# Optimization experiments

Hardware: AMD Instinct MI355X
Metric: run time of the kernel (lower is better)

## Reference

```python
import jax, jax.numpy as jnp
import numpy as np

B, S, H = 2, 2048, 2048
NH, G = 16, 4
HD = H // NH          # 128
REP = NH // G         # 4 query heads per KV group
KV = G * HD           # 512


def setup_inputs() -> dict:
    key = jax.random.key(0)
    ks = jax.random.split(key, 10)
    s = 0.02
    X = jax.random.normal(ks[0], (B, S, H), dtype=jnp.float32)
    Wq = jax.random.normal(ks[1], (H, H), dtype=jnp.float32) * s
    bq = jnp.zeros((H,), dtype=jnp.float32)
    Wk = jax.random.normal(ks[2], (H, KV), dtype=jnp.float32) * s
    bk = jnp.zeros((KV,), dtype=jnp.float32)
    Wv = jax.random.normal(ks[3], (H, KV), dtype=jnp.float32) * s
    bv = jnp.zeros((KV,), dtype=jnp.float32)
    Wo = jax.random.normal(ks[4], (H, H), dtype=jnp.float32) * s
    bo = jnp.zeros((H,), dtype=jnp.float32)
    # causal mask: 1 where attention is disallowed (strict upper triangle)
    casual_mask = jnp.triu(jnp.ones((S, S), dtype=jnp.float32), k=1)[None, None]
    return {"X": X, "Wq": Wq, "bq": bq, "Wk": Wk, "bk": bk,
            "Wv": Wv, "bv": bv, "Wo": Wo, "bo": bo,
            "casual_mask": casual_mask}


def reference(X, Wq, bq, Wk, bk, Wv, bv, Wo, bo, casual_mask):
    # projections
    q = X @ Wq + bq                          # [B,S,H]
    k = X @ Wk + bk                          # [B,S,G*HD]
    v = X @ Wv + bv                          # [B,S,G*HD]
    # split heads; q grouped as (group, rep) to match torch expand ordering
    q = q.reshape(B, S, NH, HD).transpose(0, 2, 1, 3)       # [B,NH,S,HD]
    q = q.reshape(B, G, REP, S, HD)                          # [B,G,REP,S,HD]
    k = k.reshape(B, S, G, HD).transpose(0, 2, 1, 3)         # [B,G,S,HD]
    v = v.reshape(B, S, G, HD).transpose(0, 2, 1, 3)         # [B,G,S,HD]
    scale = 1.0 / jnp.sqrt(jnp.float32(HD))
    scores = jnp.einsum('bgrqd,bgkd->bgrqk', q, k) * scale   # [B,G,REP,S,S]
    scores = scores + casual_mask * (-1e9)
    probs = jax.nn.softmax(scores, axis=-1)
    out = jnp.einsum('bgrqk,bgkd->bgrqd', probs, v)          # [B,G,REP,S,HD]
    out = out.reshape(B, NH, S, HD).transpose(0, 2, 1, 3).reshape(B, S, H)
    return out @ Wo + bo
```

## Files before the change

kernel.cpp:

```cpp
#include <hip/hip_runtime.h>

#define B_   2
#define S_   2048
#define H_   2048
#define NH_  16
#define G_   4
#define HD_  128
#define KV_  512
#define HQKV 3072

typedef __attribute__((ext_vector_type(8))) short bf16x8;
typedef __attribute__((ext_vector_type(4))) float f32x4;

__device__ __forceinline__ unsigned short f2bf(float f) {
    unsigned u = __float_as_uint(f);
    u += 0x7fff + ((u >> 16) & 1);
    return (unsigned short)(u >> 16);
}
__device__ __forceinline__ float bf2f(unsigned short s) {
    return __uint_as_float(((unsigned)s) << 16);
}

#define GLDS16(gsrc, ldst)                                                            \
    __builtin_amdgcn_global_load_lds(                                                 \
        (const __attribute__((address_space(1))) void*)(gsrc),                        \
        (__attribute__((address_space(3))) void*)(ldst), 16, 0, 0)

#define SC2F (0.08838834764831843f * 1.4426950408889634f)

__global__ void k_cvt_bf16(const float* __restrict__ in, unsigned short* __restrict__ out, int n4) {
    int i = blockIdx.x * blockDim.x + threadIdx.x;
    if (i >= n4) return;
    float4 v = ((const float4*)in)[i];
    ushort4 o;
    o.x = f2bf(v.x); o.y = f2bf(v.y); o.z = f2bf(v.z); o.w = f2bf(v.w);
    ((ushort4*)out)[i] = o;
}

__global__ void k_transpose_cvt(const float* __restrict__ in, unsigned short* __restrict__ out,
                                int R, int C) {
    __shared__ float t[32][33];
    int c0 = blockIdx.x * 32, r0 = blockIdx.y * 32;
    int tx = threadIdx.x, ty = threadIdx.y;
#pragma unroll
    for (int i = 0; i < 4; ++i)
        t[ty + i*8][tx] = in[(size_t)(r0 + ty + i*8) * C + c0 + tx];
    __syncthreads();
#pragma unroll
    for (int i = 0; i < 4; ++i)
        out[(size_t)(c0 + ty + i*8) * R + r0 + tx] = f2bf(t[tx][ty + i*8]);
}

__global__ void k_concat_bias(const float* __restrict__ bq, const float* __restrict__ bk,
                              const float* __restrict__ bv, float* __restrict__ out) {
    int i = blockIdx.x * 256 + threadIdx.x;
    if (i >= HQKV) return;
    out[i] = (i < H_) ? bq[i] : (i < H_ + KV_ ? bk[i - H_] : bv[i - H_ - KV_]);
}

__global__ void k_transpose_v(const unsigned short* __restrict__ in, unsigned short* __restrict__ out) {
    __shared__ unsigned short t[32][33];
    int b = blockIdx.z;
    int c0 = blockIdx.x * 32, s0 = blockIdx.y * 32;
    int tx = threadIdx.x, ty = threadIdx.y;
#pragma unroll
    for (int i = 0; i < 4; ++i)
        t[ty + i*8][tx] = in[((size_t)b * S_ + s0 + ty + i*8) * HQKV + (H_ + KV_) + c0 + tx];
    __syncthreads();
#pragma unroll
    for (int i = 0; i < 4; ++i)
        out[((size_t)b * KV_ + c0 + ty + i*8) * S_ + s0 + tx] = t[tx][ty + i*8];
}

template <bool BF16OUT, bool QSCALE>
__global__ __launch_bounds__(256) void k_gemm_bt(
    const unsigned short* __restrict__ A, const unsigned short* __restrict__ Bt,
    const float* __restrict__ bias, void* __restrict__ Cout, int M, int N, int K) {
    __shared__ __align__(16) unsigned short As[128 * 64];
    __shared__ __align__(16) unsigned short Bs[128 * 64];
    const int tid = threadIdx.x, lane = tid & 63, w = tid >> 6;
    const int l15 = lane & 15, l4 = lane >> 4;
    const int wr = w >> 1, wc = w & 1;
    const int m0 = blockIdx.x * 128, n0 = blockIdx.y * 128;
    f32x4 acc[4][4] = {};

    for (int kt = 0; kt < K; kt += 64) {
        __syncthreads();
#pragma unroll
        for (int i = 0; i < 4; ++i) {
            int p = (w * 4 + i) * 64 + lane;
            int row = p >> 3, c = (p & 7) ^ (row & 7);
            GLDS16(A + (size_t)(m0 + row) * K + kt + c * 8, As + (size_t)(w * 4 + i) * 512);
        }
#pragma unroll
        for (int i = 0; i < 4; ++i) {
            int p = (w * 4 + i) * 64 + lane;
            int row = p >> 3, c = (p & 7) ^ (row & 7);
            GLDS16(Bt + (size_t)(n0 + row) * K + kt + c * 8, Bs + (size_t)(w * 4 + i) * 512);
        }
        __syncthreads();
#pragma unroll
        for (int ks = 0; ks < 2; ++ks) {
            bf16x8 af[4], bfr[4];
#pragma unroll
            for (int m = 0; m < 4; ++m) {
                int row = wr * 64 + m * 16 + l15;
                int ch = (ks * 4 + l4) ^ (row & 7);
                af[m] = *(const bf16x8*)(As + row * 64 + ch * 8);
            }
#pragma unroll
            for (int n = 0; n < 4; ++n) {
                int row = wc * 64 + n * 16 + l15;
                int ch = (ks * 4 + l4) ^ (row & 7);
                bfr[n] = *(const bf16x8*)(Bs + row * 64 + ch * 8);
            }
#pragma unroll
            for (int m = 0; m < 4; ++m)
#pragma unroll
                for (int n = 0; n < 4; ++n)
                    acc[m][n] = __builtin_amdgcn_mfma_f32_16x16x32_bf16(af[m], bfr[n], acc[m][n], 0, 0, 0);
        }
    }
#pragma unroll
    for (int m = 0; m < 4; ++m) {
        int row = m0 + wr * 64 + m * 16 + l4 * 4;
#pragma unroll
        for (int n = 0; n < 4; ++n) {
            int col = n0 + wc * 64 + n * 16 + l15;
            float bv = bias[col];
#pragma unroll
            for (int r = 0; r < 4; ++r) {
                float v = acc[m][n][r] + bv;
                if (QSCALE) { if (col < H_) v *= SC2F; }
                if (BF16OUT)
                    ((unsigned short*)Cout)[(size_t)(row + r) * N + col] = f2bf(v);
                else
                    ((float*)Cout)[(size_t)(row + r) * N + col] = v;
            }
        }
    }
}

__global__ __launch_bounds__(256, 4) void k_flash(
    const unsigned short* __restrict__ QKV,
    const unsigned short* __restrict__ VT,
    unsigned short* __restrict__ Oa,
    unsigned short* __restrict__ part1,
    float* __restrict__ mlbuf) {
    __shared__ __align__(16) unsigned short Ks[64 * 128];
    __shared__ __align__(16) unsigned short Vs[128 * 64];
    __shared__ __align__(16) unsigned short Ps[4][16][36];
    const int tid = threadIdx.x, lane = tid & 63, w = tid >> 6;
    const int l15 = lane & 15, l4 = lane >> 4;
    const int bid = blockIdx.x;
    const int xcd = bid & 7, idx = bid >> 3;
    const int bh = xcd * 4 + (idx & 3);
    const int jidx = idx >> 2;
    const int b = bh >> 4, nh = bh & 15, g = nh >> 2;

    int qt, t0, t1, mode;
    if (jidx < 16) { qt = 16 + jidx; t0 = 0; t1 = 16; mode = 1; }
    else {
        int k = jidx - 16, j = k >> 1;
        if ((k & 1) == 0) { qt = 31 - j; t0 = 16; t1 = qt + 1; mode = 2; }
        else              { qt = 15 - j; t0 = 0;  t1 = qt + 1; mode = 0; }
    }
    const int qbase = qt * 64 + w * 16;

    const unsigned short* kgbase = QKV + (size_t)b * S_ * HQKV + H_ + g * HD_;
    const unsigned short* vgbase = VT + ((size_t)b * KV_ + g * HD_) * S_;

    auto issueK = [&](int kt) {
        const int kv0 = kt * 64;
#pragma unroll
        for (int i = 0; i < 4; ++i) {
            int p = i * 256 + tid;
            int row = p >> 4, c = (p & 15) ^ (row & 15);
            GLDS16(kgbase + (size_t)(kv0 + row) * HQKV + c * 8, &Ks[(i * 256 + w * 64) * 8]);
        }
    };
    auto issueV = [&](int kt) {
        const int kv0 = kt * 64;
#pragma unroll
        for (int i = 0; i < 4; ++i) {
            int p = i * 256 + tid;
            int row = p >> 3, c = (p & 7) ^ (row & 7);
            GLDS16(vgbase + (size_t)row * S_ + kv0 + c * 8, &Vs[(i * 256 + w * 64) * 8]);
        }
    };

    bf16x8 qf[4];
#pragma unroll
    for (int kb = 0; kb < 4; ++kb)
        qf[kb] = *(const bf16x8*)(QKV + (size_t)(b * S_ + qbase + l15) * HQKV +
                                  nh * HD_ + kb * 32 + l4 * 8);

    f32x4 o[8] = {};
    float mrow[4], lrow[4];
#pragma unroll
    for (int r = 0; r < 4; ++r) { mrow[r] = -1e30f; lrow[r] = 0.f; }

    issueK(t0);
    issueV(t0);

    for (int kt = t0; kt < t1; ++kt) {
        const int kv0 = kt * 64;
        asm volatile("s_waitcnt vmcnt(4)" ::: "memory");
        __builtin_amdgcn_s_barrier();
        __builtin_amdgcn_sched_barrier(0);

        f32x4 s[4] = {};
#pragma unroll
        for (int kb = 0; kb < 4; ++kb) {
            bf16x8 kf[4];
#pragma unroll
            for (int n = 0; n < 4; ++n) {
                int row = n * 16 + l15;
                int sl = (kb * 4 + l4) ^ (row & 15);
                kf[n] = *(const bf16x8*)(&Ks[(row * 16 + sl) * 8]);
            }
#pragma unroll
            for (int n = 0; n < 4; ++n)
                s[n] = __builtin_amdgcn_mfma_f32_16x16x32_bf16(qf[kb], kf[n], s[n], 0, 0, 0);
        }
        if (kv0 + 63 > qbase) {
#pragma unroll
            for (int n = 0; n < 4; ++n)
#pragma unroll
                for (int r = 0; r < 4; ++r) {
                    int kcol = kv0 + n * 16 + l15;
                    int qrow = qbase + l4 * 4 + r;
                    if (kcol > qrow) s[n][r] = -1e30f;
                }
        }
        float vm[4];
#pragma unroll
        for (int r = 0; r < 4; ++r) {
            float v = fmaxf(fmaxf(s[0][r], s[1][r]), fmaxf(s[2][r], s[3][r]));
            v = fmaxf(v, __shfl_xor(v, 1));
            v = fmaxf(v, __shfl_xor(v, 2));
            v = fmaxf(v, __shfl_xor(v, 4));
            v = fmaxf(v, __shfl_xor(v, 8));
            vm[r] = v;
        }
        int needs = 0;
#pragma unroll
        for (int r = 0; r < 4; ++r) needs |= (vm[r] > mrow[r] + 8.0f) ? 1 : 0;
        if (__any(needs)) {
            float sf[4];
#pragma unroll
            for (int r = 0; r < 4; ++r) {
                float mn = fmaxf(mrow[r], vm[r]);
                sf[r] = exp2f(mrow[r] - mn);
                mrow[r] = mn;
                lrow[r] *= sf[r];
            }
#pragma unroll
            for (int nc = 0; nc < 8; ++nc) {
                f32x4 t = o[nc];
                t[0] *= sf[0]; t[1] *= sf[1]; t[2] *= sf[2]; t[3] *= sf[3];
                o[nc] = t;
            }
        }
        float rs[4] = {0.f, 0.f, 0.f, 0.f};
#pragma unroll
        for (int n = 0; n < 4; ++n)
#pragma unroll
            for (int r = 0; r < 4; ++r) {
                float p = exp2f(s[n][r] - mrow[r]);
                s[n][r] = p;
                rs[r] += p;
            }
#pragma unroll
        for (int r = 0; r < 4; ++r) {
            float t = rs[r];
            t += __shfl_xor(t, 1); t += __shfl_xor(t, 2);
            t += __shfl_xor(t, 4); t += __shfl_xor(t, 8);
            lrow[r] += t;
        }

        asm volatile("s_waitcnt vmcnt(0)" ::: "memory");
        __builtin_amdgcn_s_barrier();
        __builtin_amdgcn_sched_barrier(0);
        if (kt + 1 < t1) issueK(kt + 1);

#pragma unroll
        for (int h = 0; h < 2; ++h) {
#pragma unroll
            for (int n = 0; n < 2; ++n)
#pragma unroll
                for (int r = 0; r < 4; ++r)
                    Ps[w][l4 * 4 + r][n * 16 + l15] = f2bf(s[2 * h + n][r]);
            bf16x8 pf = *(const bf16x8*)(&Ps[w][l15][l4 * 8]);
#pragma unroll
            for (int nc = 0; nc < 8; ++nc) {
                int row = nc * 16 + l15;
                int sl = (h * 4 + l4) ^ (row & 7);
                bf16x8 vf = *(const bf16x8*)(&Vs[(row * 8 + sl) * 8]);
                o[nc] = __builtin_amdgcn_mfma_f32_16x16x32_bf16(pf, vf, o[nc], 0, 0, 0);
            }
        }

        __builtin_amdgcn_s_barrier();
        __builtin_amdgcn_sched_barrier(0);
        if (kt + 1 < t1) issueV(kt + 1);
    }

    if (mode == 0) {
#pragma unroll
        for (int r = 0; r < 4; ++r) {
            float inv = 1.0f / lrow[r];
            int qrow = qbase + l4 * 4 + r;
            size_t base = (size_t)(b * S_ + qrow) * H_ + nh * HD_;
#pragma unroll
            for (int nc = 0; nc < 8; ++nc)
                Oa[base + nc * 16 + l15] = f2bf(o[nc][r] * inv);
        }
    } else {
        const int base = bh * 16 + (qt - 16);
        const int c = (mode == 1) ? 0 : 1;
        float* mlrec = mlbuf + (size_t)(base * 2 + c) * 64 * 2;
        if (l15 == 0) {
#pragma unroll
            for (int r = 0; r < 4; ++r) {
                int row = w * 16 + l4 * 4 + r;
                mlrec[row * 2 + 0] = mrow[r];
                mlrec[row * 2 + 1] = lrow[r];
            }
        }
        if (mode == 1) {
#pragma unroll
            for (int r = 0; r < 4; ++r) {
                int qrow = qbase + l4 * 4 + r;
                size_t ob = (size_t)(b * S_ + qrow) * H_ + nh * HD_;
#pragma unroll
                for (int nc = 0; nc < 8; ++nc)
                    Oa[ob + nc * 16 + l15] = f2bf(o[nc][r]);
            }
        } else {
#pragma unroll
            for (int r = 0; r < 4; ++r) {
                size_t pb = ((size_t)base * 64 + w * 16 + l4 * 4 + r) * 128;
#pragma unroll
                for (int nc = 0; nc < 8; ++nc)
                    part1[pb + nc * 16 + l15] = f2bf(o[nc][r]);
            }
        }
    }
}

__global__ __launch_bounds__(256) void k_combine(
    const float* __restrict__ mlbuf, const unsigned short* __restrict__ part1,
    unsigned short* __restrict__ Oa) {
    int rec = blockIdx.x;
    int bh = rec >> 4, qt = 16 + (rec & 15);
    int b = bh >> 4, nh = bh & 15;
    int row = threadIdx.x >> 2;
    int dseg = (threadIdx.x & 3) * 32;
    const float* ml0 = mlbuf + (size_t)(rec * 2 + 0) * 128;
    const float* ml1 = mlbuf + (size_t)(rec * 2 + 1) * 128;
    float m0 = ml0[row * 2], l0 = ml0[row * 2 + 1];
    float m1 = ml1[row * 2], l1 = ml1[row * 2 + 1];
    float M = fmaxf(m0, m1);
    float a0 = exp2f(m0 - M), a1 = exp2f(m1 - M);
    float L = a0 * l0 + a1 * l1;
    float s0 = a0 / L, s1 = a1 / L;
    size_t ob = ((size_t)(b * S_) + qt * 64 + row) * H_ + nh * HD_ + dseg;
    const unsigned short* p1 = part1 + ((size_t)rec * 64 + row) * 128 + dseg;
#pragma unroll
    for (int i = 0; i < 4; ++i) {
        bf16x8 v0 = *(const bf16x8*)(Oa + ob + i * 8);
        bf16x8 v1 = *(const bf16x8*)(p1 + i * 8);
        bf16x8 oo;
#pragma unroll
        for (int e = 0; e < 8; ++e)
            oo[e] = (short)f2bf(bf2f((unsigned short)v0[e]) * s0 +
                                bf2f((unsigned short)v1[e]) * s1);
        *(bf16x8*)(Oa + ob + i * 8) = oo;
    }
}

extern "C" void kernel_launch(void* const* d_in, const int* in_sizes, int n_in,
                              void* d_out, int out_size, void* d_ws, size_t ws_size,
                              hipStream_t stream) {
    const float* X  = (const float*)d_in[0];
    const float* Wq = (const float*)d_in[1];
    const float* bq = (const float*)d_in[2];
    const float* Wk = (const float*)d_in[3];
    const float* bk = (const float*)d_in[4];
    const float* Wv = (const float*)d_in[5];
    const float* bv = (const float*)d_in[6];
    const float* Wo = (const float*)d_in[7];
    const float* bo = (const float*)d_in[8];
    float* out = (float*)d_out;

    if (ws_size < 80000000) return;
    char* ws = (char*)d_ws;
    unsigned short* Xb    = (unsigned short*)(ws);
    unsigned short* WqkvT = (unsigned short*)(ws + 16777216);
    unsigned short* WoT   = (unsigned short*)(ws + 29360128);
    unsigned short* QKV   = (unsigned short*)(ws + 37748736);
    unsigned short* VbT   = (unsigned short*)(ws + 62914560);
    unsigned short* part1 = (unsigned short*)(ws + 67108864);
    float*          mlbuf = (float*)(ws + 75497472);
    float*          bqkv  = (float*)(ws + 76021760);
    unsigned short* AOb   = Xb;

    k_cvt_bf16<<<(B_ * S_ * H_ / 4 + 255) / 256, 256, 0, stream>>>(X, Xb, B_ * S_ * H_ / 4);
    k_transpose_cvt<<<dim3(H_ / 32, H_ / 32), dim3(32, 8), 0, stream>>>(Wq, WqkvT, H_, H_);
    k_transpose_cvt<<<dim3(KV_ / 32, H_ / 32), dim3(32, 8), 0, stream>>>(Wk, WqkvT + (size_t)H_ * H_, H_, KV_);
    k_transpose_cvt<<<dim3(KV_ / 32, H_ / 32), dim3(32, 8), 0, stream>>>(Wv, WqkvT + (size_t)(H_ + KV_) * H_, H_, KV_);
    k_transpose_cvt<<<dim3(H_ / 32, H_ / 32), dim3(32, 8), 0, stream>>>(Wo, WoT, H_, H_);
    k_concat_bias<<<(HQKV + 255) / 256, 256, 0, stream>>>(bq, bk, bv, bqkv);

    k_gemm_bt<true, true><<<dim3(32, 24), 256, 0, stream>>>(Xb, WqkvT, bqkv, QKV, 4096, HQKV, 2048);

    k_transpose_v<<<dim3(KV_ / 32, S_ / 32, B_), dim3(32, 8), 0, stream>>>(QKV, VbT);
    k_flash<<<dim3(1536), 256, 0, stream>>>(QKV, VbT, AOb, part1, mlbuf);
    k_combine<<<dim3(512), 256, 0, stream>>>(mlbuf, part1, AOb);

    k_gemm_bt<false, false><<<dim3(32, 16), 256, 0, stream>>>(AOb, WoT, bo, out, 4096, 2048, 2048);
}
```

Baseline: 236.6 us.

## Transpose flash MFMA operands to keep P in registers and drop LDS staging

```diff
diff --git a/kernel.cpp b/kernel.cpp
--- a/kernel.cpp
+++ b/kernel.cpp
@@ -20,6 +20,11 @@
 __device__ __forceinline__ float bf2f(unsigned short s) {
     return __uint_as_float(((unsigned)s) << 16);
 }
+__device__ __forceinline__ unsigned cvtpk(float a, float b) {
+    unsigned r;
+    asm volatile("v_cvt_pk_bf16_f32 %0, %1, %2" : "=v"(r) : "v"(a), "v"(b));
+    return r;
+}
 
 #define GLDS16(gsrc, ldst)                                                            \
     __builtin_amdgcn_global_load_lds(                                                 \
@@ -49,6 +54,25 @@
 #pragma unroll
     for (int i = 0; i < 4; ++i)
         out[(size_t)(c0 + ty + i*8) * R + r0 + tx] = f2bf(t[tx][ty + i*8]);
+}
+
+__global__ void k_transpose_qkv(const float* __restrict__ Wq, const float* __restrict__ Wk,
+                                const float* __restrict__ Wv, unsigned short* __restrict__ out) {
+    __shared__ float t[32][33];
+    int n0g = blockIdx.x * 32;
+    int h0 = blockIdx.y * 32;
+    const float* src; int C, n0l;
+    if (n0g < H_)            { src = Wq; C = H_;  n0l = n0g; }
+    else if (n0g < H_ + KV_) { src = Wk; C = KV_; n0l = n0g - H_; }
+    else                     { src = Wv; C = KV_; n0l = n0g - H_ - KV_; }
+    int tx = threadIdx.x, ty = threadIdx.y;
+#pragma unroll
+    for (int i = 0; i < 4; ++i)
+        t[ty + i*8][tx] = src[(size_t)(h0 + ty + i*8) * C + n0l + tx];
+    __syncthreads();
+#pragma unroll
+    for (int i = 0; i < 4; ++i)
+        out[(size_t)(n0g + ty + i*8) * H_ + h0 + tx] = f2bf(t[tx][ty + i*8]);
 }
 
 __global__ void k_concat_bias(const float* __restrict__ bq, const float* __restrict__ bk,
@@ -149,7 +173,6 @@
     float* __restrict__ mlbuf) {
     __shared__ __align__(16) unsigned short Ks[64 * 128];
     __shared__ __align__(16) unsigned short Vs[128 * 64];
-    __shared__ __align__(16) unsigned short Ps[4][16][36];
     const int tid = threadIdx.x, lane = tid & 63, w = tid >> 6;
     const int l15 = lane & 15, l4 = lane >> 4;
     const int bid = blockIdx.x;
@@ -196,9 +219,11 @@
                                   nh * HD_ + kb * 32 + l4 * 8);
 
     f32x4 o[8] = {};
-    float mrow[4], lrow[4];
-#pragma unroll
-    for (int r = 0; r < 4; ++r) { mrow[r] = -1e30f; lrow[r] = 0.f; }
+    float m_r = -1e30f, l_r = 0.f;
+
+    const int src0 = l15 + 16 * ((2 * l4) & 3);
+    const int src1 = l15 + 16 * ((2 * l4 + 1) & 3);
+    const bool hsel = ((l4 >> 1) & 1) != 0;
 
     issueK(t0);
     issueV(t0);
@@ -219,64 +244,59 @@
                 int sl = (kb * 4 + l4) ^ (row & 15);
                 kf[n] = *(const bf16x8*)(&Ks[(row * 16 + sl) * 8]);
             }
+            __builtin_amdgcn_s_setprio(1);
 #pragma unroll
             for (int n = 0; n < 4; ++n)
-                s[n] = __builtin_amdgcn_mfma_f32_16x16x32_bf16(qf[kb], kf[n], s[n], 0, 0, 0);
+                s[n] = __builtin_amdgcn_mfma_f32_16x16x32_bf16(kf[n], qf[kb], s[n], 0, 0, 0);
+            __builtin_amdgcn_s_setprio(0);
         }
         if (kv0 + 63 > qbase) {
+            const int qrow = qbase + l15;
 #pragma unroll
             for (int n = 0; n < 4; ++n)
 #pragma unroll
                 for (int r = 0; r < 4; ++r) {
-                    int kcol = kv0 + n * 16 + l15;
-                    int qrow = qbase + l4 * 4 + r;
+                    int kcol = kv0 + n * 16 + l4 * 4 + r;
                     if (kcol > qrow) s[n][r] = -1e30f;
                 }
         }
-        float vm[4];
-#pragma unroll
-        for (int r = 0; r < 4; ++r) {
-            float v = fmaxf(fmaxf(s[0][r], s[1][r]), fmaxf(s[2][r], s[3][r]));
-            v = fmaxf(v, __shfl_xor(v, 1));
-            v = fmaxf(v, __shfl_xor(v, 2));
-            v = fmaxf(v, __shfl_xor(v, 4));
-            v = fmaxf(v, __shfl_xor(v, 8));
-            vm[r] = v;
-        }
-        int needs = 0;
-#pragma unroll
-        for (int r = 0; r < 4; ++r) needs |= (vm[r] > mrow[r] + 8.0f) ? 1 : 0;
-        if (__any(needs)) {
-            float sf[4];
-#pragma unroll
-            for (int r = 0; r < 4; ++r) {
-                float mn = fmaxf(mrow[r], vm[r]);
-                sf[r] = exp2f(mrow[r] - mn);
-                mrow[r] = mn;
-                lrow[r] *= sf[r];
-            }
+        float pmax = s[0][0];
+#pragma unroll
+        for (int n = 0; n < 4; ++n)
+#pragma unroll
+            for (int r = 0; r < 4; ++r) pmax = fmaxf(pmax, s[n][r]);
+        pmax = fmaxf(pmax, __shfl_xor(pmax, 16));
+        pmax = fmaxf(pmax, __shfl_xor(pmax, 32));
+        if (__any(pmax > m_r + 8.0f)) {
+            float mn = fmaxf(m_r, pmax);
+            float sf = exp2f(m_r - mn);
+            m_r = mn;
+            l_r *= sf;
 #pragma unroll
             for (int nc = 0; nc < 8; ++nc) {
                 f32x4 t = o[nc];
-                t[0] *= sf[0]; t[1] *= sf[1]; t[2] *= sf[2]; t[3] *= sf[3];
+                t[0] *= sf; t[1] *= sf; t[2] *= sf; t[3] *= sf;
                 o[nc] = t;
             }
         }
-        float rs[4] = {0.f, 0.f, 0.f, 0.f};
+        float rsum = 0.f;
 #pragma unroll
         for (int n = 0; n < 4; ++n)
 #pragma unroll
             for (int r = 0; r < 4; ++r) {
-                float p = exp2f(s[n][r] - mrow[r]);
+                float p = exp2f(s[n][r] - m_r);
                 s[n][r] = p;
-                rs[r] += p;
-            }
-#pragma unroll
-        for (int r = 0; r < 4; ++r) {
-            float t = rs[r];
-            t += __shfl_xor(t, 1); t += __shfl_xor(t, 2);
-            t += __shfl_xor(t, 4); t += __shfl_xor(t, 8);
-            lrow[r] += t;
+                rsum += p;
+            }
+        rsum += __shfl_xor(rsum, 16);
+        rsum += __shfl_xor(rsum, 32);
+        l_r += rsum;
+
+        unsigned plo[4], phi[4];
+#pragma unroll
+        for (int n = 0; n < 4; ++n) {
+            plo[n] = cvtpk(s[n][0], s[n][1]);
+            phi[n] = cvtpk(s[n][2], s[n][3]);
         }
 
         asm volatile("s_waitcnt vmcnt(0)" ::: "memory");
@@ -285,20 +305,24 @@
         if (kt + 1 < t1) issueK(kt + 1);
 
 #pragma unroll
-        for (int h = 0; h < 2; ++h) {
-#pragma unroll
-            for (int n = 0; n < 2; ++n)
-#pragma unroll
-                for (int r = 0; r < 4; ++r)
-                    Ps[w][l4 * 4 + r][n * 16 + l15] = f2bf(s[2 * h + n][r]);
-            bf16x8 pf = *(const bf16x8*)(&Ps[w][l15][l4 * 8]);
+        for (int kb = 0; kb < 2; ++kb) {
+            const int n0i = 2 * kb, n1i = 2 * kb + 1;
+            unsigned a0, a1, w0, w1, w2, w3;
+            a0 = __shfl((int)plo[n0i], src0); a1 = __shfl((int)plo[n1i], src0); w0 = hsel ? a1 : a0;
+            a0 = __shfl((int)phi[n0i], src0); a1 = __shfl((int)phi[n1i], src0); w1 = hsel ? a1 : a0;
+            a0 = __shfl((int)plo[n0i], src1); a1 = __shfl((int)plo[n1i], src1); w2 = hsel ? a1 : a0;
+            a0 = __shfl((int)phi[n0i], src1); a1 = __shfl((int)phi[n1i], src1); w3 = hsel ? a1 : a0;
+            int4 pw = make_int4((int)w0, (int)w1, (int)w2, (int)w3);
+            bf16x8 pf = *(bf16x8*)&pw;
+            __builtin_amdgcn_s_setprio(1);
 #pragma unroll
             for (int nc = 0; nc < 8; ++nc) {
                 int row = nc * 16 + l15;
-                int sl = (h * 4 + l4) ^ (row & 7);
+                int sl = (kb * 4 + l4) ^ (row & 7);
                 bf16x8 vf = *(const bf16x8*)(&Vs[(row * 8 + sl) * 8]);
-                o[nc] = __builtin_amdgcn_mfma_f32_16x16x32_bf16(pf, vf, o[nc], 0, 0, 0);
-            }
+                o[nc] = __builtin_amdgcn_mfma_f32_16x16x32_bf16(vf, pf, o[nc], 0, 0, 0);
+            }
+            __builtin_amdgcn_s_setprio(0);
         }
 
         __builtin_amdgcn_s_barrier();
@@ -306,44 +330,43 @@
         if (kt + 1 < t1) issueV(kt + 1);
     }
 
+    const int qrow = qbase + l15;
     if (mode == 0) {
-#pragma unroll
-        for (int r = 0; r < 4; ++r) {
-            float inv = 1.0f / lrow[r];
-            int qrow = qbase + l4 * 4 + r;
-            size_t base = (size_t)(b * S_ + qrow) * H_ + nh * HD_;
-#pragma unroll
-            for (int nc = 0; nc < 8; ++nc)
-                Oa[base + nc * 16 + l15] = f2bf(o[nc][r] * inv);
+        float inv = 1.0f / l_r;
+        size_t base = (size_t)(b * S_ + qrow) * H_ + nh * HD_ + l4 * 4;
+#pragma unroll
+        for (int nc = 0; nc < 8; ++nc) {
+            uint2 pk;
+            pk.x = cvtpk(o[nc][0] * inv, o[nc][1] * inv);
+            pk.y = cvtpk(o[nc][2] * inv, o[nc][3] * inv);
+            *(uint2*)(Oa + base + nc * 16) = pk;
         }
     } else {
         const int base = bh * 16 + (qt - 16);
         const int c = (mode == 1) ? 0 : 1;
         float* mlrec = mlbuf + (size_t)(base * 2 + c) * 64 * 2;
-        if (l15 == 0) {
-#pragma unroll
-            for (int r = 0; r < 4; ++r) {
-                int row = w * 16 + l4 * 4 + r;
-                mlrec[row * 2 + 0] = mrow[r];
-                mlrec[row * 2 + 1] = lrow[r];
-            }
+        if (l4 == 0) {
+            int row = w * 16 + l15;
+            mlrec[row * 2 + 0] = m_r;
+            mlrec[row * 2 + 1] = l_r;
         }
         if (mode == 1) {
-#pragma unroll
-            for (int r = 0; r < 4; ++r) {
-                int qrow = qbase + l4 * 4 + r;
-                size_t ob = (size_t)(b * S_ + qrow) * H_ + nh * HD_;
-#pragma unroll
-                for (int nc = 0; nc < 8; ++nc)
-                    Oa[ob + nc * 16 + l15] = f2bf(o[nc][r]);
+            size_t ob = (size_t)(b * S_ + qrow) * H_ + nh * HD_ + l4 * 4;
+#pragma unroll
+            for (int nc = 0; nc < 8; ++nc) {
+                uint2 pk;
+                pk.x = cvtpk(o[nc][0], o[nc][1]);
+                pk.y = cvtpk(o[nc][2], o[nc][3]);
+                *(uint2*)(Oa + ob + nc * 16) = pk;
             }
         } else {
-#pragma unroll
-            for (int r = 0; r < 4; ++r) {
-                size_t pb = ((size_t)base * 64 + w * 16 + l4 * 4 + r) * 128;
-#pragma unroll
-                for (int nc = 0; nc < 8; ++nc)
-                    part1[pb + nc * 16 + l15] = f2bf(o[nc][r]);
+            size_t pb = ((size_t)base * 64 + w * 16 + l15) * 128 + l4 * 4;
+#pragma unroll
+            for (int nc = 0; nc < 8; ++nc) {
+                uint2 pk;
+                pk.x = cvtpk(o[nc][0], o[nc][1]);
+                pk.y = cvtpk(o[nc][2], o[nc][3]);
+                *(uint2*)(part1 + pb + nc * 16) = pk;
             }
         }
     }
@@ -407,9 +430,7 @@
     unsigned short* AOb   = Xb;
 
     k_cvt_bf16<<<(B_ * S_ * H_ / 4 + 255) / 256, 256, 0, stream>>>(X, Xb, B_ * S_ * H_ / 4);
-    k_transpose_cvt<<<dim3(H_ / 32, H_ / 32), dim3(32, 8), 0, stream>>>(Wq, WqkvT, H_, H_);
-    k_transpose_cvt<<<dim3(KV_ / 32, H_ / 32), dim3(32, 8), 0, stream>>>(Wk, WqkvT + (size_t)H_ * H_, H_, KV_);
-    k_transpose_cvt<<<dim3(KV_ / 32, H_ / 32), dim3(32, 8), 0, stream>>>(Wv, WqkvT + (size_t)(H_ + KV_) * H_, H_, KV_);
+    k_transpose_qkv<<<dim3(HQKV / 32, H_ / 32), dim3(32, 8), 0, stream>>>(Wq, Wk, Wv, WqkvT);
     k_transpose_cvt<<<dim3(H_ / 32, H_ / 32), dim3(32, 8), 0, stream>>>(Wo, WoT, H_, H_);
     k_concat_bias<<<(HQKV + 255) / 256, 256, 0, stream>>>(bq, bk, bv, bqkv);
 
```

Result: faster. 221.3 us (-6.5%).
